# Optimization experiments

Hardware: AMD Instinct MI355X
Metric: run time of the kernel (lower is better)

Reference implementation:

```python
import jax, jax.numpy as jnp
import numpy as np

B, M = 512, 2048            # batch of src-tgt pairs, sampled walk positions per pair
NUM_KEYS = 1_000_000        # unique (node, time) keys in nodetime2emb map
NUM_NODES = 100_000
LP = 4                      # num_layers + 1 (saw encoding width)
ENC = 32                    # enc_dim
FEAT = 64                   # node feature dim (MergeLayer dim2)
D3, D4 = 64, 1              # MergeLayer hidden / output dims


def setup_inputs() -> dict:
    key = jax.random.key(0)
    ks = jax.random.split(key, 12)
    s = 0.05
    return {
        "pos_table": jax.random.uniform(ks[0], (NUM_KEYS, LP), dtype=jnp.float32),
        "node_feat": jax.random.normal(ks[1], (NUM_NODES, FEAT), dtype=jnp.float32),
        "W1": jax.random.normal(ks[2], (LP, ENC), dtype=jnp.float32) * s,
        "b1": jnp.zeros((ENC,), dtype=jnp.float32),
        "W2": jax.random.normal(ks[3], (ENC, ENC), dtype=jnp.float32) * s,
        "b2": jnp.zeros((ENC,), dtype=jnp.float32),
        "Wm1": jax.random.normal(ks[4], (ENC + FEAT, D3), dtype=jnp.float32) * s,
        "bm1": jnp.zeros((D3,), dtype=jnp.float32),
        "Wm2": jax.random.normal(ks[5], (D3, D4), dtype=jnp.float32) * s,
        "bm2": jnp.zeros((D4,), dtype=jnp.float32),
        "key_idx": jax.random.randint(ks[6], (B, M), 0, NUM_KEYS, dtype=jnp.int32),
        "node_idx": jax.random.randint(ks[7], (B, M), 0, NUM_NODES, dtype=jnp.int32),
    }


def reference(pos_table, node_feat, W1, b1, W2, b2, Wm1, bm1, Wm2, bm2, key_idx, node_idx):
    # PositionEncoder.forward: gather saw encodings by (node, time) key,
    # then trainable_embedding = Linear(LP->ENC) -> ReLU -> Linear(ENC->ENC)
    enc = pos_table[key_idx]                       # [B, M, LP] irregular gather
    pe = jax.nn.relu(enc @ W1 + b1) @ W2 + b2      # [B, M, ENC]
    # gather raw node features for the same walk positions
    feat = node_feat[node_idx]                     # [B, M, FEAT] irregular gather
    # MergeLayer (non_linear=True): concat -> fc1 -> ReLU -> fc2
    x = jnp.concatenate([pe, feat], axis=-1)       # [B, M, ENC+FEAT]
    z = jax.nn.relu(x @ Wm1 + bm1) @ Wm2 + bm2     # [B, M, 1]
    return z
```

## Files before the change

kernel.cpp:

```cpp
#include <hip/hip_runtime.h>


typedef _Float16 half8 __attribute__((ext_vector_type(8)));
typedef float floatx4 __attribute__((ext_vector_type(4)));

#define HSTR 40
#define WSTR 104

__global__ __launch_bounds__(256, 2) void neurtw_mfma(
    const float* __restrict__ pos_table,
    const float* __restrict__ node_feat,
    const float* __restrict__ W1,
    const float* __restrict__ b1,
    const float* __restrict__ W2,
    const float* __restrict__ b2,
    const float* __restrict__ Wm1,
    const float* __restrict__ bm1,
    const float* __restrict__ Wm2,
    const float* __restrict__ bm2,
    const int*   __restrict__ key_idx,
    const int*   __restrict__ node_idx,
    float*       __restrict__ out)
{
    __shared__ _Float16 h_lds[256 * HSTR];
    __shared__ _Float16 pe_lds[256 * HSTR];
    __shared__ _Float16 w2t[32 * HSTR];
    __shared__ _Float16 wm1t[64 * WSTR];
    __shared__ int nd_lds[256];

    const int tid = threadIdx.x;
    const int blockBase = blockIdx.x * 256;
    const int row = blockBase + tid;

    #pragma unroll
    for (int i = 0; i < 24; ++i) {
        const int idx = i * 256 + tid;
        const int k = idx >> 6, n = idx & 63;
        wm1t[n * WSTR + k] = (_Float16)Wm1[idx];
    }
    #pragma unroll
    for (int i = 0; i < 4; ++i) {
        const int idx = i * 256 + tid;
        const int k = idx >> 5, n = idx & 31;
        w2t[n * HSTR + k] = (_Float16)W2[idx];
    }

    nd_lds[tid] = node_idx[row];
    const int kk = key_idx[row];
    const float4 enc = *(const float4*)(pos_table + (size_t)kk * 4);

    {
        #pragma unroll
        for (int g = 0; g < 4; ++g) {
            half8 hv;
            #pragma unroll
            for (int j8 = 0; j8 < 8; ++j8) {
                const int j = g * 8 + j8;
                float a = fmaf(enc.w, W1[96 + j],
                          fmaf(enc.z, W1[64 + j],
                          fmaf(enc.y, W1[32 + j],
                          fmaf(enc.x, W1[j], b1[j]))));
                hv[j8] = (_Float16)fmaxf(a, 0.0f);
            }
            *(half8*)(&h_lds[tid * HSTR + g * 8]) = hv;
        }
    }
    __syncthreads();

    const int lane = tid & 63;
    const int r0 = (tid >> 6) * 64;
    const int ln = lane & 15;
    const int q  = lane >> 4;

    {
        half8 a_h[4];
        #pragma unroll
        for (int rt = 0; rt < 4; ++rt)
            a_h[rt] = *(const half8*)(&h_lds[(r0 + rt * 16 + ln) * HSTR + q * 8]);
        half8 b_w2[2];
        #pragma unroll
        for (int ct = 0; ct < 2; ++ct)
            b_w2[ct] = *(const half8*)(&w2t[(ct * 16 + ln) * HSTR + q * 8]);

        const float b2v0 = b2[ln], b2v1 = b2[16 + ln];

        #pragma unroll
        for (int rt = 0; rt < 4; ++rt) {
            #pragma unroll
            for (int ct = 0; ct < 2; ++ct) {
                floatx4 c = {0.f, 0.f, 0.f, 0.f};
                c = __builtin_amdgcn_mfma_f32_16x16x32_f16(a_h[rt], b_w2[ct], c, 0, 0, 0);
                const float bb = ct ? b2v1 : b2v0;
                #pragma unroll
                for (int r = 0; r < 4; ++r)
                    pe_lds[(r0 + rt * 16 + q * 4 + r) * HSTR + ct * 16 + ln] =
                        (_Float16)(c[r] + bb);
            }
        }
    }
    __syncthreads();

    floatx4 acc[4][4];
    {
        float4 fr[4][2][2];
        #pragma unroll
        for (int rt = 0; rt < 4; ++rt) {
            const int rowl = r0 + rt * 16 + ln;
            const int ndm = nd_lds[rowl];
            const float* fb = node_feat + (size_t)ndm * 64 + q * 8;
            #pragma unroll
            for (int kt = 0; kt < 2; ++kt) {
                fr[rt][kt][0] = *(const float4*)(fb + kt * 32);
                fr[rt][kt][1] = *(const float4*)(fb + kt * 32 + 4);
            }
        }

        #pragma unroll
        for (int ct = 0; ct < 4; ++ct) {
            const float bb = bm1[ct * 16 + ln];
            #pragma unroll
            for (int rt = 0; rt < 4; ++rt)
                acc[rt][ct] = (floatx4){bb, bb, bb, bb};
        }

        {
            half8 a_pe[4];
            #pragma unroll
            for (int rt = 0; rt < 4; ++rt)
                a_pe[rt] = *(const half8*)(&pe_lds[(r0 + rt * 16 + ln) * HSTR + q * 8]);
            half8 b0[4];
            #pragma unroll
            for (int ct = 0; ct < 4; ++ct)
                b0[ct] = *(const half8*)(&wm1t[(ct * 16 + ln) * WSTR + q * 8]);
            #pragma unroll
            for (int rt = 0; rt < 4; ++rt)
                #pragma unroll
                for (int ct = 0; ct < 4; ++ct)
                    acc[rt][ct] = __builtin_amdgcn_mfma_f32_16x16x32_f16(
                        a_pe[rt], b0[ct], acc[rt][ct], 0, 0, 0);
        }

        #pragma unroll
        for (int kt = 0; kt < 2; ++kt) {
            half8 bk[4];
            #pragma unroll
            for (int ct = 0; ct < 4; ++ct)
                bk[ct] = *(const half8*)(&wm1t[(ct * 16 + ln) * WSTR + 32 + kt * 32 + q * 8]);
            #pragma unroll
            for (int rt = 0; rt < 4; ++rt) {
                half8 ak;
                const float4 lo = fr[rt][kt][0], hi = fr[rt][kt][1];
                ak[0] = (_Float16)lo.x; ak[1] = (_Float16)lo.y;
                ak[2] = (_Float16)lo.z; ak[3] = (_Float16)lo.w;
                ak[4] = (_Float16)hi.x; ak[5] = (_Float16)hi.y;
                ak[6] = (_Float16)hi.z; ak[7] = (_Float16)hi.w;
                #pragma unroll
                for (int ct = 0; ct < 4; ++ct)
                    acc[rt][ct] = __builtin_amdgcn_mfma_f32_16x16x32_f16(
                        ak, bk[ct], acc[rt][ct], 0, 0, 0);
            }
        }
    }

    {
        float wm2v[4];
        #pragma unroll
        for (int ct = 0; ct < 4; ++ct) wm2v[ct] = Wm2[ct * 16 + ln];
        const float bm2s = bm2[0];

        #pragma unroll
        for (int rt = 0; rt < 4; ++rt) {
            #pragma unroll
            for (int r = 0; r < 4; ++r) {
                float p = 0.0f;
                #pragma unroll
                for (int ct = 0; ct < 4; ++ct)
                    p = fmaf(fmaxf(acc[rt][ct][r], 0.0f), wm2v[ct], p);
                p += __shfl_xor(p, 1);
                p += __shfl_xor(p, 2);
                p += __shfl_xor(p, 4);
                p += __shfl_xor(p, 8);
                if (ln == 0)
                    out[blockBase + r0 + rt * 16 + q * 4 + r] = p + bm2s;
            }
        }
    }
}

extern "C" void kernel_launch(void* const* d_in, const int* in_sizes, int n_in,
                              void* d_out, int out_size, void* d_ws, size_t ws_size,
                              hipStream_t stream) {
    const float* pos_table = (const float*)d_in[0];
    const float* node_feat = (const float*)d_in[1];
    const float* W1        = (const float*)d_in[2];
    const float* b1        = (const float*)d_in[3];
    const float* W2        = (const float*)d_in[4];
    const float* b2        = (const float*)d_in[5];
    const float* Wm1       = (const float*)d_in[6];
    const float* bm1       = (const float*)d_in[7];
    const float* Wm2       = (const float*)d_in[8];
    const float* bm2       = (const float*)d_in[9];
    const int*   key_idx   = (const int*)d_in[10];
    const int*   node_idx  = (const int*)d_in[11];
    float* out = (float*)d_out;

    const int rows = in_sizes[10];
    const int grid = rows / 256;
    neurtw_mfma<<<grid, 256, 0, stream>>>(
        pos_table, node_feat, W1, b1, W2, b2, Wm1, bm1, Wm2, bm2,
        key_idx, node_idx, out);
}
```

Baseline: 174.3 us.

## Pre-convert node features to fp16 and use persistent grid-stride blocks

Adds a pre-pass kernel that converts the node feature table to fp16 in workspace, so the main kernel's random gathers read half the bytes per row. The main kernel becomes persistent with a fixed grid looping over row tiles, loading weights once per block into registers/LDS. It also merges the h/pe LDS buffers, keeps W2 in registers, and raises occupancy to 3 blocks per CU. The conversion pass costs an extra full-table read and write every call (about 38 MB of traffic), which may offset the smaller gathers.

Result: faster. 158.9 us (-8.9%).

```diff
diff --git a/kernel.cpp b/kernel.cpp
--- a/kernel.cpp
+++ b/kernel.cpp
@@ -6,8 +6,23 @@
 
 #define HSTR 40
 #define WSTR 104
-
-__global__ __launch_bounds__(256, 2) void neurtw_mfma(
+#define GRID 768
+
+__global__ void feat_to_f16(const float* __restrict__ nf,
+                            _Float16* __restrict__ o, int n8) {
+    int t = blockIdx.x * 256 + threadIdx.x;
+    if (t >= n8) return;
+    const float4* p = (const float4*)nf + (size_t)t * 2;
+    const float4 a = p[0], b = p[1];
+    half8 h;
+    h[0] = (_Float16)a.x; h[1] = (_Float16)a.y;
+    h[2] = (_Float16)a.z; h[3] = (_Float16)a.w;
+    h[4] = (_Float16)b.x; h[5] = (_Float16)b.y;
+    h[6] = (_Float16)b.z; h[7] = (_Float16)b.w;
+    *((half8*)o + t) = h;
+}
+
+__global__ __launch_bounds__(256, 3) void neurtw_mfma(
     const float* __restrict__ pos_table,
     const float* __restrict__ node_feat,
     const float* __restrict__ W1,
@@ -20,36 +35,86 @@
     const float* __restrict__ bm2,
     const int*   __restrict__ key_idx,
     const int*   __restrict__ node_idx,
-    float*       __restrict__ out)
+    const _Float16* __restrict__ feat16,
+    int use_f16,
+    float*       __restrict__ out,
+    int rows)
 {
-    __shared__ _Float16 h_lds[256 * HSTR];
-    __shared__ _Float16 pe_lds[256 * HSTR];
-    __shared__ _Float16 w2t[32 * HSTR];
+    __shared__ _Float16 hpe[256 * HSTR];
     __shared__ _Float16 wm1t[64 * WSTR];
-    __shared__ int nd_lds[256];
-
-    const int tid = threadIdx.x;
-    const int blockBase = blockIdx.x * 256;
-    const int row = blockBase + tid;
+
+    const int tid  = threadIdx.x;
+    const int lane = tid & 63;
+    const int r0   = (tid >> 6) * 64;
+    const int ln   = lane & 15;
+    const int q    = lane >> 4;
 
     #pragma unroll
-    for (int i = 0; i < 24; ++i) {
-        const int idx = i * 256 + tid;
-        const int k = idx >> 6, n = idx & 63;
-        wm1t[n * WSTR + k] = (_Float16)Wm1[idx];
-    }
+    for (int i = 0; i < 3; ++i) {
+        const int task = i * 256 + tid;
+        const int n = task & 63, k8 = task >> 6;
+        half8 w;
+        #pragma unroll
+        for (int kk = 0; kk < 8; ++kk)
+            w[kk] = (_Float16)Wm1[(k8 * 8 + kk) * 64 + n];
+        *(half8*)(&wm1t[n * WSTR + k8 * 8]) = w;
+    }
+
+    half8 b_w2[2];
     #pragma unroll
-    for (int i = 0; i < 4; ++i) {
-        const int idx = i * 256 + tid;
-        const int k = idx >> 5, n = idx & 31;
-        w2t[n * HSTR + k] = (_Float16)W2[idx];
-    }
-
-    nd_lds[tid] = node_idx[row];
-    const int kk = key_idx[row];
-    const float4 enc = *(const float4*)(pos_table + (size_t)kk * 4);
-
-    {
+    for (int ct = 0; ct < 2; ++ct)
+        #pragma unroll
+        for (int j = 0; j < 8; ++j)
+            b_w2[ct][j] = (_Float16)W2[(q * 8 + j) * 32 + ct * 16 + ln];
+    float b2v[2];
+    b2v[0] = b2[ln]; b2v[1] = b2[16 + ln];
+    float bm1v[4], wm2v[4];
+    #pragma unroll
+    for (int ct = 0; ct < 4; ++ct) {
+        bm1v[ct] = bm1[ct * 16 + ln];
+        wm2v[ct] = Wm2[ct * 16 + ln];
+    }
+    const float bm2s = bm2[0];
+
+    __syncthreads();
+
+    for (int base = blockIdx.x * 256; base < rows; base += GRID * 256) {
+        const int row = base + tid;
+
+        int ndr[4];
+        #pragma unroll
+        for (int rt = 0; rt < 4; ++rt)
+            ndr[rt] = node_idx[base + r0 + rt * 16 + ln];
+
+        half8 fA[4][2];
+        if (use_f16) {
+            #pragma unroll
+            for (int rt = 0; rt < 4; ++rt) {
+                const _Float16* fb = feat16 + (size_t)ndr[rt] * 64 + q * 8;
+                fA[rt][0] = *(const half8*)(fb);
+                fA[rt][1] = *(const half8*)(fb + 32);
+            }
+        } else {
+            #pragma unroll
+            for (int rt = 0; rt < 4; ++rt) {
+                const float* fb = node_feat + (size_t)ndr[rt] * 64 + q * 8;
+                #pragma unroll
+                for (int kt = 0; kt < 2; ++kt) {
+                    const float4 lo = *(const float4*)(fb + kt * 32);
+                    const float4 hi = *(const float4*)(fb + kt * 32 + 4);
+                    half8 h;
+                    h[0] = (_Float16)lo.x; h[1] = (_Float16)lo.y;
+                    h[2] = (_Float16)lo.z; h[3] = (_Float16)lo.w;
+                    h[4] = (_Float16)hi.x; h[5] = (_Float16)hi.y;
+                    h[6] = (_Float16)hi.z; h[7] = (_Float16)hi.w;
+                    fA[rt][kt] = h;
+                }
+            }
+        }
+
+        const int kk = key_idx[row];
+        const float4 enc = *(const float4*)(pos_table + (size_t)kk * 4);
+
         #pragma unroll
         for (int g = 0; g < 4; ++g) {
             half8 hv;
@@ -62,62 +127,39 @@
                           fmaf(enc.x, W1[j], b1[j]))));
                 hv[j8] = (_Float16)fmaxf(a, 0.0f);
             }
-            *(half8*)(&h_lds[tid * HSTR + g * 8]) = hv;
-        }
-    }
-    __syncthreads();
-
-    const int lane = tid & 63;
-    const int r0 = (tid >> 6) * 64;
-    const int ln = lane & 15;
-    const int q  = lane >> 4;
-
-    {
+            *(half8*)(&hpe[tid * HSTR + g * 8]) = hv;
+        }
+        __syncthreads();
+
         half8 a_h[4];
         #pragma unroll
         for (int rt = 0; rt < 4; ++rt)
-            a_h[rt] = *(const half8*)(&h_lds[(r0 + rt * 16 + ln) * HSTR + q * 8]);
-        half8 b_w2[2];
-        #pragma unroll
-        for (int ct = 0; ct < 2; ++ct)
-            b_w2[ct] = *(const half8*)(&w2t[(ct * 16 + ln) * HSTR + q * 8]);
-
-        const float b2v0 = b2[ln], b2v1 = b2[16 + ln];
-
-        #pragma unroll
-        for (int rt = 0; rt < 4; ++rt) {
+            a_h[rt] = *(const half8*)(&hpe[(r0 + rt * 16 + ln) * HSTR + q * 8]);
+
+        floatx4 pc[4][2];
+        #pragma unroll
+        for (int rt = 0; rt < 4; ++rt)
             #pragma unroll
             for (int ct = 0; ct < 2; ++ct) {
                 floatx4 c = {0.f, 0.f, 0.f, 0.f};
-                c = __builtin_amdgcn_mfma_f32_16x16x32_f16(a_h[rt], b_w2[ct], c, 0, 0, 0);
-                const float bb = ct ? b2v1 : b2v0;
+                pc[rt][ct] = __builtin_amdgcn_mfma_f32_16x16x32_f16(
+                    a_h[rt], b_w2[ct], c, 0, 0, 0);
+            }
+
+        #pragma unroll
+        for (int rt = 0; rt < 4; ++rt)
+            #pragma unroll
+            for (int ct = 0; ct < 2; ++ct)
                 #pragma unroll
                 for (int r = 0; r < 4; ++r)
-                    pe_lds[(r0 + rt * 16 + q * 4 + r) * HSTR + ct * 16 + ln] =
-                        (_Float16)(c[r] + bb);
-            }
-        }
-    }
-    __syncthreads();
-
-    floatx4 acc[4][4];
-    {
-        float4 fr[4][2][2];
-        #pragma unroll
-        for (int rt = 0; rt < 4; ++rt) {
-            const int rowl = r0 + rt * 16 + ln;
-            const int ndm = nd_lds[rowl];
-            const float* fb = node_feat + (size_t)ndm * 64 + q * 8;
-            #pragma unroll
-            for (int kt = 0; kt < 2; ++kt) {
-                fr[rt][kt][0] = *(const float4*)(fb + kt * 32);
-                fr[rt][kt][1] = *(const float4*)(fb + kt * 32 + 4);
-            }
-        }
-
+                    hpe[(r0 + rt * 16 + q * 4 + r) * HSTR + ct * 16 + ln] =
+                        (_Float16)(pc[rt][ct][r] + b2v[ct]);
+        __syncthreads();
+
+        floatx4 acc[4][4];
         #pragma unroll
         for (int ct = 0; ct < 4; ++ct) {
-            const float bb = bm1[ct * 16 + ln];
+            const float bb = bm1v[ct];
             #pragma unroll
             for (int rt = 0; rt < 4; ++rt)
                 acc[rt][ct] = (floatx4){bb, bb, bb, bb};
@@ -127,7 +169,7 @@
             half8 a_pe[4];
             #pragma unroll
             for (int rt = 0; rt < 4; ++rt)
-                a_pe[rt] = *(const half8*)(&pe_lds[(r0 + rt * 16 + ln) * HSTR + q * 8]);
+                a_pe[rt] = *(const half8*)(&hpe[(r0 + rt * 16 + ln) * HSTR + q * 8]);
             half8 b0[4];
             #pragma unroll
             for (int ct = 0; ct < 4; ++ct)
@@ -147,26 +189,12 @@
             for (int ct = 0; ct < 4; ++ct)
                 bk[ct] = *(const half8*)(&wm1t[(ct * 16 + ln) * WSTR + 32 + kt * 32 + q * 8]);
             #pragma unroll
-            for (int rt = 0; rt < 4; ++rt) {
-                half8 ak;
-                const float4 lo = fr[rt][kt][0], hi = fr[rt][kt][1];
-                ak[0] = (_Float16)lo.x; ak[1] = (_Float16)lo.y;
-                ak[2] = (_Float16)lo.z; ak[3] = (_Float16)lo.w;
-                ak[4] = (_Float16)hi.x; ak[5] = (_Float16)hi.y;
-                ak[6] = (_Float16)hi.z; ak[7] = (_Float16)hi.w;
+            for (int rt = 0; rt < 4; ++rt)
                 #pragma unroll
                 for (int ct = 0; ct < 4; ++ct)
                     acc[rt][ct] = __builtin_amdgcn_mfma_f32_16x16x32_f16(
-                        ak, bk[ct], acc[rt][ct], 0, 0, 0);
-            }
-        }
-    }
-
-    {
-        float wm2v[4];
-        #pragma unroll
-        for (int ct = 0; ct < 4; ++ct) wm2v[ct] = Wm2[ct * 16 + ln];
-        const float bm2s = bm2[0];
+                        fA[rt][kt], bk[ct], acc[rt][ct], 0, 0, 0);
+        }
 
         #pragma unroll
         for (int rt = 0; rt < 4; ++rt) {
@@ -181,7 +209,7 @@
                 p += __shfl_xor(p, 4);
                 p += __shfl_xor(p, 8);
                 if (ln == 0)
-                    out[blockBase + r0 + rt * 16 + q * 4 + r] = p + bm2s;
+                    out[base + r0 + rt * 16 + q * 4 + r] = p + bm2s;
             }
         }
     }
@@ -205,8 +233,17 @@
     float* out = (float*)d_out;
 
     const int rows = in_sizes[10];
-    const int grid = rows / 256;
-    neurtw_mfma<<<grid, 256, 0, stream>>>(
+    const int nfeat = in_sizes[1];
+    const size_t need = (size_t)nfeat * sizeof(_Float16);
+    const int use_f16 = (ws_size >= need) ? 1 : 0;
+
+    if (use_f16) {
+        const int n8 = nfeat / 8;
+        feat_to_f16<<<(n8 + 255) / 256, 256, 0, stream>>>(
+            node_feat, (_Float16*)d_ws, n8);
+    }
+
+    neurtw_mfma<<<GRID, 256, 0, stream>>>(
         pos_table, node_feat, W1, b1, W2, b2, Wm1, bm1, Wm2, bm2,
-        key_idx, node_idx, out);
+        key_idx, node_idx, (const _Float16*)d_ws, use_f16, out, rows);
 }
```
